# Kernel optimization log

Measured on AMD Instinct MI355X. Metric: run time of the kernel, lower is better.

## Reference

```python
import jax, jax.numpy as jnp
import numpy as np

FEATURES = 1024
EXPANDED = 16
HIDDEN = FEATURES * EXPANDED  # 16384
BATCH = 4096


def setup_inputs() -> dict:
    key = jax.random.key(0)
    k_x, k_we, k_be, k_wd, k_bd = jax.random.split(key, 5)
    s_enc = 1.0 / np.sqrt(FEATURES)
    s_dec = 1.0 / np.sqrt(HIDDEN)
    return {
        "x": jax.random.normal(k_x, (BATCH, FEATURES), dtype=jnp.float32),
        "W_enc": jax.random.uniform(k_we, (HIDDEN, FEATURES), jnp.float32, -s_enc, s_enc),
        "b_enc": jax.random.uniform(k_be, (HIDDEN,), jnp.float32, -s_enc, s_enc),
        "W_dec": jax.random.uniform(k_wd, (FEATURES, HIDDEN), jnp.float32, -s_dec, s_dec),
        "b_dec": jax.random.uniform(k_bd, (FEATURES,), jnp.float32, -s_dec, s_dec),
        "activate": 64,
    }


def reference(x, W_enc, b_enc, W_dec, b_dec, activate):
    # Encoder: subtract decoder bias, dense GEMM -> pre-activations a [B, HIDDEN]
    xbar = x - b_dec
    a = jnp.einsum("bf,hf->bh", xbar, W_enc) + b_enc
    # TopK per row, relu values, scatter back into a zero tensor
    vals, idx = jax.lax.top_k(a, activate)           # [B, k]
    f = jnp.zeros_like(a)
    rows = jnp.arange(a.shape[0])[:, None]           # [B, 1]
    f = f.at[rows, idx].set(jax.nn.relu(vals))
    # Decoder: dense GEMM back to feature space (faithful to original dense decode)
    xhat = jnp.einsum("bh,fh->bf", f, W_dec) + b_dec
    return f, xhat
```

## Files before the change

kernel.cpp:

```cpp
#include <hip/hip_runtime.h>
#include <cstdint>

#define B_ 4096
#define F_ 1024
#define H_ 16384
#define TOPK 64
#define MAXC 192
#define TWOE 0.020f

typedef unsigned short u16;
typedef __attribute__((ext_vector_type(8))) _Float16 f16x8;
typedef __attribute__((ext_vector_type(8))) unsigned short u16x8;
typedef __attribute__((ext_vector_type(4))) float f32x4;

__device__ __forceinline__ u16 f2bf(float f) {
  union { float f; uint32_t u; } v; v.f = f;
  uint32_t u = v.u;
  uint32_t r = u + 0x7FFFu + ((u >> 16) & 1u);
  return (u16)(r >> 16);
}
__device__ __forceinline__ float bf2f(u16 h) {
  union { uint32_t u; float f; } v; v.u = ((uint32_t)h) << 16; return v.f;
}
__device__ __forceinline__ u16 f2h(float f) {
  union { _Float16 h; u16 u; } v; v.h = (_Float16)f; return v.u;
}
__device__ __forceinline__ float h2f(u16 h) {
  union { _Float16 h; u16 u; } v; v.u = h; return (float)v.h;
}
__device__ __forceinline__ uint32_t key2(uint32_t v) {
  uint32_t s = (v >> 15) & 0x00010001u;
  return v & ~(s * 0xFFFFu);
}

__device__ __forceinline__ void async16(const void* g, void* l) {
  __builtin_amdgcn_global_load_lds(
      reinterpret_cast<const __attribute__((address_space(1))) uint32_t*>(
          reinterpret_cast<uintptr_t>(g)),
      reinterpret_cast<__attribute__((address_space(3))) uint32_t*>(
          reinterpret_cast<uintptr_t>(l)),
      16, 0, 0);
}

__global__ __launch_bounds__(256) void k_xbar(const float* __restrict__ x,
                                              const float* __restrict__ b_dec,
                                              u16* __restrict__ xbar) {
  int i = blockIdx.x * 256 + threadIdx.x;
  int base = i * 4;
  int col = base & (F_ - 1);
  float4 xv = *(const float4*)(x + base);
  float4 bv = *(const float4*)(b_dec + col);
  ushort4 o;
  o.x = f2h(xv.x - bv.x); o.y = f2h(xv.y - bv.y);
  o.z = f2h(xv.z - bv.z); o.w = f2h(xv.w - bv.w);
  *(ushort4*)(xbar + base) = o;
}

__global__ __launch_bounds__(256) void k_cast(const float* __restrict__ src,
                                              u16* __restrict__ dst) {
  size_t base = (size_t)(blockIdx.x * 256 + threadIdx.x) * 4;
  float4 v = *(const float4*)(src + base);
  ushort4 o; o.x = f2h(v.x); o.y = f2h(v.y); o.z = f2h(v.z); o.w = f2h(v.w);
  *(ushort4*)(dst + base) = o;
}

__global__ __launch_bounds__(256) void k_transpose(const float* __restrict__ Wdec,
                                                   u16* __restrict__ WdecT) {
  __shared__ float tile[32][33];
  int hb = blockIdx.x * 32, fb = blockIdx.y * 32;
  int tx = threadIdx.x & 31, ty = threadIdx.x >> 5;
#pragma unroll
  for (int i = 0; i < 32; i += 8)
    tile[ty + i][tx] = Wdec[(size_t)(fb + ty + i) * H_ + hb + tx];
  __syncthreads();
#pragma unroll
  for (int i = 0; i < 32; i += 8)
    WdecT[(size_t)(hb + ty + i) * F_ + fb + tx] = f2bf(tile[tx][ty + i]);
}

__device__ __forceinline__ void gemm_step(const u16* __restrict__ bA,
                                          const u16* __restrict__ bB,
                                          int aoff, int boff, int kcp,
                                          f32x4 (&acc)[4][4]) {
  f16x8 av[4], bv[4];
#pragma unroll
  for (int i = 0; i < 4; ++i)
    av[i] = *(const f16x8*)&bA[(aoff + i * 16) * 32 + kcp];
#pragma unroll
  for (int j = 0; j < 4; ++j)
    bv[j] = *(const f16x8*)&bB[(boff + j * 16) * 32 + kcp];
#pragma unroll
  for (int i = 0; i < 4; ++i)
#pragma unroll
    for (int j = 0; j < 4; ++j)
      acc[i][j] = __builtin_amdgcn_mfma_f32_16x16x32_f16(av[i], bv[j], acc[i][j], 0, 0, 0);
}

__global__ __launch_bounds__(256) void k_gemm(const u16* __restrict__ A,
                                              const u16* __restrict__ Bm,
                                              const float* __restrict__ b_enc,
                                              u16* __restrict__ Cf16) {
  __shared__ u16 lA[2][128 * 32];
  __shared__ u16 lB[2][128 * 32];
  const int tid = threadIdx.x;
  const int lane = tid & 63, wave = tid >> 6;
  const int wm = wave >> 1, wn = wave & 1;
  const int bx = blockIdx.x, by = blockIdx.y;

  const int kcs = (tid & 3) ^ ((tid >> 3) & 3);
  const u16* gA0 = A + (size_t)(by * 128 + (tid >> 2)) * F_ + kcs * 8;
  const u16* gA1 = gA0 + 64 * F_;
  const u16* gB0 = Bm + (size_t)(bx * 128 + (tid >> 2)) * F_ + kcs * 8;
  const u16* gB1 = gB0 + 64 * F_;

#define STAGE(b_, k0_)                          \
  {                                             \
    async16(gA0 + (k0_), &lA[b_][tid * 8]);     \
    async16(gA1 + (k0_), &lA[b_][tid * 8 + 2048]); \
    async16(gB0 + (k0_), &lB[b_][tid * 8]);     \
    async16(gB1 + (k0_), &lB[b_][tid * 8 + 2048]); \
  }

  f32x4 acc[4][4] = {};
  const int lm = lane & 15;
  const int kcp = (((lane >> 4) ^ ((lm >> 1) & 3))) * 8;
  const int aoff = wm * 64 + lm, boff = wn * 64 + lm;

  STAGE(0, 0);
  __syncthreads();
#pragma unroll
  for (int t = 0; t < 31; ++t) {
    if ((t & 1) == 0) {
      STAGE(1, (t + 1) * 32);
      gemm_step(lA[0], lB[0], aoff, boff, kcp, acc);
    } else {
      STAGE(0, (t + 1) * 32);
      gemm_step(lA[1], lB[1], aoff, boff, kcp, acc);
    }
    __syncthreads();
  }
  gemm_step(lA[1], lB[1], aoff, boff, kcp, acc);
#undef STAGE

#pragma unroll
  for (int i = 0; i < 4; ++i) {
    int rowg = by * 128 + wm * 64 + i * 16 + (lane >> 4) * 4;
#pragma unroll
    for (int j = 0; j < 4; ++j) {
      int colg = bx * 128 + wn * 64 + j * 16 + lm;
      float be = b_enc[colg];
      u16* cp = Cf16 + (size_t)rowg * H_ + colg;
#pragma unroll
      for (int r = 0; r < 4; ++r)
        cp[(size_t)r * H_] = f2h(acc[i][j][r] + be);
    }
  }
}

__global__ __launch_bounds__(256) void k_selrefdec(const u16* __restrict__ af16,
                                                   const float* __restrict__ x,
                                                   const float* __restrict__ b_dec,
                                                   const float* __restrict__ Wenc,
                                                   const float* __restrict__ b_enc,
                                                   const u16* __restrict__ WdecT,
                                                   float* __restrict__ f,
                                                   float* __restrict__ xhat,
                                                   int* __restrict__ decIdx,
                                                   float* __restrict__ decVal) {
  const int row = blockIdx.x, tid = threadIdx.x;
  const int lane = tid & 63, wave = tid >> 6;
  __shared__ float wbuf[4][2][F_];
  __shared__ float xs[F_];
  __shared__ double vals[MAXC];
  __shared__ float bes[MAXC];
  __shared__ int idxs[MAXC];
  __shared__ int fIdx[TOPK];
  __shared__ float fVal[TOPK];
  __shared__ int s_cnt8[2][4];
  __shared__ int s_sure, s_amb;

  if (tid == 0) { s_sure = 0; s_amb = 0; idxs[0] = 0; }
  if (tid < TOPK) { fIdx[tid] = 0; fVal[tid] = 0.f; }
  for (int k = tid; k < F_; k += 256)
    xs[k] = x[(size_t)row * F_ + k] - b_dec[k];

  float* frow = f + (size_t)row * H_;
  if (row < B_ / 2) {
    const f32x4 z4 = {0.f, 0.f, 0.f, 0.f};
    for (int i = tid; i < H_ / 4; i += 256)
      __builtin_nontemporal_store(z4, (f32x4*)frow + i);
  }

  uint32_t pr[32];
  {
    const uint4* arow16 = (const uint4*)(af16 + (size_t)row * H_);
#pragma unroll
    for (int j = 0; j < 8; ++j) {
      uint4 v = arow16[tid + 256 * j];
      pr[j * 4 + 0] = key2(v.x);
      pr[j * 4 + 1] = key2(v.y);
      pr[j * 4 + 2] = key2(v.z);
      pr[j * 4 + 3] = key2(v.w);
    }
  }

  uint32_t lo = 0, hi = 0x7C00;
  int it = 0;
  while (hi - lo > 1) {
    const uint32_t mid = (lo + hi) >> 1;
    int c = 0;
#pragma unroll
    for (int r = 0; r < 32; ++r) {
      c += ((pr[r] & 0xFFFFu) >= mid);
      c += ((pr[r] >> 16) >= mid);
    }
#pragma unroll
    for (int off = 32; off > 0; off >>= 1) c += __shfl_xor(c, off);
    if (lane == 0) s_cnt8[it & 1][wave] = c;
    __syncthreads();
    const int* scp = s_cnt8[it & 1];
    const int tot = scp[0] + scp[1] + scp[2] + scp[3];
    if (tot >= TOPK) lo = mid; else hi = mid;
    ++it;
  }
  const float v64f = h2f((u16)lo);
  const float sc = v64f + TWOE;
  const float al = v64f - TWOE;

#pragma unroll
  for (int j = 0; j < 8; ++j) {
#pragma unroll
    for (int w = 0; w < 4; ++w) {
      const uint32_t v = pr[j * 4 + w];
      const int ib = (tid + 256 * j) * 8 + w * 2;
      const float f0 = h2f((u16)(v & 0xFFFFu));
      const float f1 = h2f((u16)(v >> 16));
      if (f0 > sc) {
        int p = atomicAdd(&s_sure, 1);
        if (p < TOPK) { fIdx[p] = ib; fVal[p] = f0 > 0.f ? f0 : 0.f; }
      } else if (f0 >= al) {
        int p = atomicAdd(&s_amb, 1);
        if (p < MAXC) idxs[p] = ib;
      }
      if (f1 > sc) {
        int p = atomicAdd(&s_sure, 1);
        if (p < TOPK) { fIdx[p] = ib + 1; fVal[p] = f1 > 0.f ? f1 : 0.f; }
      } else if (f1 >= al) {
        int p = atomicAdd(&s_amb, 1);
        if (p < MAXC) idxs[p] = ib + 1;
      }
    }
  }
  __syncthreads();
  const int S = s_sure < TOPK ? s_sure : TOPK;
  const int cnt = s_amb < MAXC ? s_amb : MAXC;
  for (int c = tid; c < cnt; c += 256) bes[c] = b_enc[idxs[c]];
  __syncthreads();

  float xr[16];
#pragma unroll
  for (int ch = 0; ch < 4; ++ch)
#pragma unroll
    for (int j = 0; j < 4; ++j)
      xr[ch * 4 + j] = xs[ch * 256 + lane * 4 + j];

#define ISSUE_ROW(c_, b_)                                                  \
  {                                                                        \
    int cc_ = (c_) < cnt ? (c_) : 0;                                       \
    const float* src_ = Wenc + (size_t)idxs[cc_] * F_ + lane * 4;          \
    float* dst_ = &wbuf[wave][(b_)][lane * 4];                             \
    async16(src_ + 0, dst_ + 0);                                           \
    async16(src_ + 256, dst_ + 256);                                       \
    async16(src_ + 512, dst_ + 512);                                       \
    async16(src_ + 768, dst_ + 768);                                       \
  }

  const int nIter = (cnt - wave + 3) / 4;
  ISSUE_ROW(wave, 0);
  ISSUE_ROW(wave + 4, 1);

  for (int i = 0; i < nIter; ++i) {
    const int c = wave + i * 4;
    const int bsel = i & 1;
    asm volatile("s_waitcnt vmcnt(4)" ::: "memory");
    __builtin_amdgcn_sched_barrier(0);

    const float4* wr = (const float4*)wbuf[wave][bsel];
    double s = 0.0;
#pragma unroll
    for (int ch = 0; ch < 4; ++ch) {
      float4 wv = wr[ch * 64 + lane];
      s = fma((double)xr[ch * 4 + 0], (double)wv.x, s);
      s = fma((double)xr[ch * 4 + 1], (double)wv.y, s);
      s = fma((double)xr[ch * 4 + 2], (double)wv.z, s);
      s = fma((double)xr[ch * 4 + 3], (double)wv.w, s);
    }
    __builtin_amdgcn_sched_barrier(0);
    ISSUE_ROW(wave + (i + 2) * 4, bsel);

#pragma unroll
    for (int off = 32; off > 0; off >>= 1) s += __shfl_xor(s, off);
    if (lane == 0 && c < cnt) vals[c] = s + (double)bes[c];
  }
#undef ISSUE_ROW
  __syncthreads();

  const int Kp = TOPK - S;
  for (int c = tid; c < cnt; c += 256) {
    const double v = vals[c];
    const int h = idxs[c];
    int rank = 0;
    for (int o = 0; o < cnt; ++o) {
      double vo = vals[o];
      rank += (vo > v) || (vo == v && idxs[o] < h);
    }
    if (rank < Kp) {
      float fv = v > 0.0 ? (float)v : 0.0f;
      fIdx[S + rank] = h;
      fVal[S + rank] = fv;
    }
  }
  __syncthreads();

  if (tid < TOPK) {
    decIdx[row * TOPK + tid] = fIdx[tid];
    decVal[row * TOPK + tid] = fVal[tid];
    if (row < B_ / 2) frow[fIdx[tid] & (H_ - 1)] = fVal[tid];
  }

  const int cb = (tid & 127) * 8;
  const int par = tid >> 7;
  float a[8] = {0.f, 0.f, 0.f, 0.f, 0.f, 0.f, 0.f, 0.f};
#pragma unroll 8
  for (int j2 = 0; j2 < TOPK / 2; ++j2) {
    const int j = j2 * 2 + par;
    const float v = fVal[j];
    const u16x8 w = *(const u16x8*)(WdecT + (size_t)(fIdx[j] & (H_ - 1)) * F_ + cb);
#pragma unroll
    for (int k = 0; k < 8; ++k) a[k] += v * bf2f(w[k]);
  }
  if (par) {
#pragma unroll
    for (int k = 0; k < 8; ++k) xs[cb + k] = a[k];
  }
  __syncthreads();
  if (!par) {
    float4 bd0 = *(const float4*)(b_dec + cb);
    float4 bd1 = *(const float4*)(b_dec + cb + 4);
    float4 o0, o1;
    o0.x = a[0] + xs[cb + 0] + bd0.x;
    o0.y = a[1] + xs[cb + 1] + bd0.y;
    o0.z = a[2] + xs[cb + 2] + bd0.z;
    o0.w = a[3] + xs[cb + 3] + bd0.w;
    o1.x = a[4] + xs[cb + 4] + bd1.x;
    o1.y = a[5] + xs[cb + 5] + bd1.y;
    o1.z = a[6] + xs[cb + 6] + bd1.z;
    o1.w = a[7] + xs[cb + 7] + bd1.w;
    float* xp = xhat + (size_t)row * F_ + cb;
    *(float4*)xp = o0;
    *(float4*)(xp + 4) = o1;
  }
}

__global__ __launch_bounds__(256) void k_zs(const int* __restrict__ decIdx,
                                            const float* __restrict__ decVal,
                                            float* __restrict__ f) {
  const int row = B_ / 2 + blockIdx.x, tid = threadIdx.x;
  float* frow = f + (size_t)row * H_;
  const f32x4 z4 = {0.f, 0.f, 0.f, 0.f};
  for (int i = tid; i < H_ / 4; i += 256)
    __builtin_nontemporal_store(z4, (f32x4*)frow + i);
  __syncthreads();
  if (tid < TOPK)
    frow[decIdx[row * TOPK + tid] & (H_ - 1)] = decVal[row * TOPK + tid];
}

extern "C" void kernel_launch(void* const* d_in, const int* in_sizes, int n_in,
                              void* d_out, int out_size, void* d_ws, size_t ws_size,
                              hipStream_t stream) {
  const float* x    = (const float*)d_in[0];
  const float* Wenc = (const float*)d_in[1];
  const float* benc = (const float*)d_in[2];
  const float* Wdec = (const float*)d_in[3];
  const float* bdec = (const float*)d_in[4];

  float* out  = (float*)d_out;
  float* f    = out;
  float* xhat = out + (size_t)B_ * H_;
  u16* af16 = (u16*)(f + (size_t)B_ * H_ / 2);

  char* ws = (char*)d_ws;
  u16*  xbar    = (u16*)ws;
  u16*  wencb   = (u16*)(ws + (size_t)(8)  * 1048576);
  u16*  wdecT   = (u16*)(ws + (size_t)(40) * 1048576);
  int*  decIdx  = (int*)(ws + (size_t)(76) * 1048576);
  float* decVal = (float*)(ws + (size_t)(77) * 1048576);

  k_xbar<<<B_ * F_ / 1024, 256, 0, stream>>>(x, bdec, xbar);
  k_cast<<<H_ * F_ / 1024, 256, 0, stream>>>(Wenc, wencb);
  k_transpose<<<dim3(H_ / 32, F_ / 32), 256, 0, stream>>>(Wdec, wdecT);
  k_gemm<<<dim3(H_ / 128, B_ / 128), 256, 0, stream>>>(xbar, wencb, benc, af16);
  k_selrefdec<<<B_, 256, 0, stream>>>(af16, x, bdec, Wenc, benc, wdecT,
                                      f, xhat, decIdx, decVal);
  k_zs<<<B_ / 2, 256, 0, stream>>>(decIdx, decVal, f);
}
```

Before: 707.9 us.

## Merge prep kernels, coarsen threshold search, use integer compares and fp16 dot2 decode

Fuses the xbar, W_enc cast and W_dec transpose into one launch to cut launch overhead and tail idle time. The top-k threshold bisection now stops at a width of 8 fp16 codes instead of 1, and candidate classification compares integer keys instead of converting to float. The decoder stores W_dec transposed as fp16 instead of bf16 and accumulates pairs of terms with packed fp16 dot2 instructions. The coarser bisection widens the ambiguous band, so more candidates go through the exact refinement path, and rounding the selected values to fp16 for fdot2 costs some precision.

```diff
diff --git a/kernel.cpp b/kernel.cpp
--- a/kernel.cpp
+++ b/kernel.cpp
@@ -8,8 +8,15 @@
 #define MAXC 192
 #define TWOE 0.020f
 
+#if defined(__has_builtin)
+#if __has_builtin(__builtin_amdgcn_fdot2)
+#define HAVE_FDOT2 1
+#endif
+#endif
+
 typedef unsigned short u16;
 typedef __attribute__((ext_vector_type(8))) _Float16 f16x8;
+typedef __attribute__((ext_vector_type(2))) _Float16 h16x2;
 typedef __attribute__((ext_vector_type(8))) unsigned short u16x8;
 typedef __attribute__((ext_vector_type(4))) float f32x4;
 
@@ -42,40 +49,42 @@
       16, 0, 0);
 }
 
-__global__ __launch_bounds__(256) void k_xbar(const float* __restrict__ x,
+__global__ __launch_bounds__(256) void k_prep(const float* __restrict__ x,
                                               const float* __restrict__ b_dec,
-                                              u16* __restrict__ xbar) {
-  int i = blockIdx.x * 256 + threadIdx.x;
-  int base = i * 4;
-  int col = base & (F_ - 1);
-  float4 xv = *(const float4*)(x + base);
-  float4 bv = *(const float4*)(b_dec + col);
-  ushort4 o;
-  o.x = f2h(xv.x - bv.x); o.y = f2h(xv.y - bv.y);
-  o.z = f2h(xv.z - bv.z); o.w = f2h(xv.w - bv.w);
-  *(ushort4*)(xbar + base) = o;
-}
-
-__global__ __launch_bounds__(256) void k_cast(const float* __restrict__ src,
-                                              u16* __restrict__ dst) {
-  size_t base = (size_t)(blockIdx.x * 256 + threadIdx.x) * 4;
-  float4 v = *(const float4*)(src + base);
-  ushort4 o; o.x = f2h(v.x); o.y = f2h(v.y); o.z = f2h(v.z); o.w = f2h(v.w);
-  *(ushort4*)(dst + base) = o;
-}
-
-__global__ __launch_bounds__(256) void k_transpose(const float* __restrict__ Wdec,
-                                                   u16* __restrict__ WdecT) {
+                                              const float* __restrict__ Wenc,
+                                              const float* __restrict__ Wdec,
+                                              u16* __restrict__ xbar,
+                                              u16* __restrict__ wencb,
+                                              u16* __restrict__ wdecT) {
   __shared__ float tile[32][33];
-  int hb = blockIdx.x * 32, fb = blockIdx.y * 32;
-  int tx = threadIdx.x & 31, ty = threadIdx.x >> 5;
-#pragma unroll
-  for (int i = 0; i < 32; i += 8)
-    tile[ty + i][tx] = Wdec[(size_t)(fb + ty + i) * H_ + hb + tx];
-  __syncthreads();
-#pragma unroll
-  for (int i = 0; i < 32; i += 8)
-    WdecT[(size_t)(hb + ty + i) * F_ + fb + tx] = f2bf(tile[tx][ty + i]);
+  const int b = blockIdx.x, tid = threadIdx.x;
+  if (b < 4096) {
+    int i = b * 256 + tid;
+    int base = i * 4;
+    int col = base & (F_ - 1);
+    float4 xv = *(const float4*)(x + base);
+    float4 bv = *(const float4*)(b_dec + col);
+    ushort4 o;
+    o.x = f2h(xv.x - bv.x); o.y = f2h(xv.y - bv.y);
+    o.z = f2h(xv.z - bv.z); o.w = f2h(xv.w - bv.w);
+    *(ushort4*)(xbar + base) = o;
+  } else if (b < 20480) {
+    size_t base = ((size_t)(b - 4096) * 256 + tid) * 4;
+    float4 v = *(const float4*)(Wenc + base);
+    ushort4 o; o.x = f2h(v.x); o.y = f2h(v.y); o.z = f2h(v.z); o.w = f2h(v.w);
+    *(ushort4*)(wencb + base) = o;
+  } else {
+    const int t = b - 20480;
+    const int hb = (t & 511) * 32, fb = (t >> 9) * 32;
+    const int tx = tid & 31, ty = tid >> 5;
+#pragma unroll
+    for (int i = 0; i < 32; i += 8)
+      tile[ty + i][tx] = Wdec[(size_t)(fb + ty + i) * H_ + hb + tx];
+    __syncthreads();
+#pragma unroll
+    for (int i = 0; i < 32; i += 8)
+      wdecT[(size_t)(hb + ty + i) * F_ + fb + tx] = f2h(tile[tx][ty + i]);
+  }
 }
 
 __device__ __forceinline__ void gemm_step(const u16* __restrict__ bA,
@@ -206,7 +215,7 @@
 
   uint32_t lo = 0, hi = 0x7C00;
   int it = 0;
-  while (hi - lo > 1) {
+  while (hi - lo > 8) {
     const uint32_t mid = (lo + hi) >> 1;
     int c = 0;
 #pragma unroll
@@ -223,9 +232,10 @@
     if (tot >= TOPK) lo = mid; else hi = mid;
     ++it;
   }
-  const float v64f = h2f((u16)lo);
-  const float sc = v64f + TWOE;
-  const float al = v64f - TWOE;
+  const float scf = h2f((u16)hi) + TWOE;
+  const float alf = h2f((u16)lo) - TWOE;
+  const int ksc = f2h(scf);
+  const int kal = (alf <= 0.f) ? 0 : (int)f2h(alf);
 
 #pragma unroll
   for (int j = 0; j < 8; ++j) {
@@ -233,19 +243,18 @@
     for (int w = 0; w < 4; ++w) {
       const uint32_t v = pr[j * 4 + w];
       const int ib = (tid + 256 * j) * 8 + w * 2;
-      const float f0 = h2f((u16)(v & 0xFFFFu));
-      const float f1 = h2f((u16)(v >> 16));
-      if (f0 > sc) {
+      const int k0 = (int)(v & 0xFFFFu), k1 = (int)(v >> 16);
+      if (k0 > ksc) {
         int p = atomicAdd(&s_sure, 1);
-        if (p < TOPK) { fIdx[p] = ib; fVal[p] = f0 > 0.f ? f0 : 0.f; }
-      } else if (f0 >= al) {
+        if (p < TOPK) { fIdx[p] = ib; fVal[p] = h2f((u16)k0); }
+      } else if (k0 >= kal) {
         int p = atomicAdd(&s_amb, 1);
         if (p < MAXC) idxs[p] = ib;
       }
-      if (f1 > sc) {
+      if (k1 > ksc) {
         int p = atomicAdd(&s_sure, 1);
-        if (p < TOPK) { fIdx[p] = ib + 1; fVal[p] = f1 > 0.f ? f1 : 0.f; }
-      } else if (f1 >= al) {
+        if (p < TOPK) { fIdx[p] = ib + 1; fVal[p] = h2f((u16)k1); }
+      } else if (k1 >= kal) {
         int p = atomicAdd(&s_amb, 1);
         if (p < MAXC) idxs[p] = ib + 1;
       }
@@ -331,13 +340,33 @@
   const int cb = (tid & 127) * 8;
   const int par = tid >> 7;
   float a[8] = {0.f, 0.f, 0.f, 0.f, 0.f, 0.f, 0.f, 0.f};
-#pragma unroll 8
-  for (int j2 = 0; j2 < TOPK / 2; ++j2) {
-    const int j = j2 * 2 + par;
-    const float v = fVal[j];
-    const u16x8 w = *(const u16x8*)(WdecT + (size_t)(fIdx[j] & (H_ - 1)) * F_ + cb);
-#pragma unroll
-    for (int k = 0; k < 8; ++k) a[k] += v * bf2f(w[k]);
+#pragma unroll 4
+  for (int m = 0; m < 16; ++m) {
+    const int j0 = 4 * m + par, j1 = j0 + 2;
+    const float v0 = fVal[j0], v1 = fVal[j1];
+    const uint4 w0 = *(const uint4*)(WdecT + (size_t)(fIdx[j0] & (H_ - 1)) * F_ + cb);
+    const uint4 w1 = *(const uint4*)(WdecT + (size_t)(fIdx[j1] & (H_ - 1)) * F_ + cb);
+#if defined(HAVE_FDOT2)
+    h16x2 vv; vv[0] = (_Float16)v0; vv[1] = (_Float16)v1;
+#pragma unroll
+    for (int q = 0; q < 4; ++q) {
+      const uint32_t x0 = ((const uint32_t*)&w0)[q];
+      const uint32_t x1 = ((const uint32_t*)&w1)[q];
+      union { uint32_t u; h16x2 h; } plo, phi;
+      plo.u = __builtin_amdgcn_perm(x1, x0, 0x05040100u);
+      phi.u = __builtin_amdgcn_perm(x1, x0, 0x07060302u);
+      a[q * 2 + 0] = __builtin_amdgcn_fdot2(plo.h, vv, a[q * 2 + 0], false);
+      a[q * 2 + 1] = __builtin_amdgcn_fdot2(phi.h, vv, a[q * 2 + 1], false);
+    }
+#else
+#pragma unroll
+    for (int q = 0; q < 4; ++q) {
+      const uint32_t x0 = ((const uint32_t*)&w0)[q];
+      const uint32_t x1 = ((const uint32_t*)&w1)[q];
+      a[q * 2 + 0] += v0 * h2f((u16)(x0 & 0xFFFFu)) + v1 * h2f((u16)(x1 & 0xFFFFu));
+      a[q * 2 + 1] += v0 * h2f((u16)(x0 >> 16)) + v1 * h2f((u16)(x1 >> 16));
+    }
+#endif
   }
   if (par) {
 #pragma unroll
@@ -396,9 +425,7 @@
   int*  decIdx  = (int*)(ws + (size_t)(76) * 1048576);
   float* decVal = (float*)(ws + (size_t)(77) * 1048576);
 
-  k_xbar<<<B_ * F_ / 1024, 256, 0, stream>>>(x, bdec, xbar);
-  k_cast<<<H_ * F_ / 1024, 256, 0, stream>>>(Wenc, wencb);
-  k_transpose<<<dim3(H_ / 32, F_ / 32), 256, 0, stream>>>(Wdec, wdecT);
+  k_prep<<<36864, 256, 0, stream>>>(x, bdec, Wenc, Wdec, xbar, wencb, wdecT);
   k_gemm<<<dim3(H_ / 128, B_ / 128), 256, 0, stream>>>(xbar, wencb, benc, af16);
   k_selrefdec<<<B_, 256, 0, stream>>>(af16, x, bdec, Wenc, benc, wdecT,
                                       f, xhat, decIdx, decVal);
```

Measured after the change: 704.9 us. Within noise of the previous version (-0.4%).
